# Kernel tuning notes

Hardware: AMD Instinct MI355X
Metric: run time of the kernel (lower is better)

The kernel has to match this reference:

```python
import jax, jax.numpy as jnp
import numpy as np

B, S_IMG, S_TXT, D, H, HD = 1, 2048, 512, 3072, 24, 128
EMB, N_IP = 4096, 64
IP_SCALE = 1.0
EPS = 1e-6
SM_SCALE = 1.0 / np.sqrt(HD).astype(np.float32)


def _lin(x, W, b=None):
    # torch Linear: y = x @ W.T + b, W: [out, in]
    y = jnp.einsum('bsd,od->bso', x, W)
    return y if b is None else y + b


def _heads(x):  # [B,S,D] -> [B,H,S,HD]
    return x.reshape(B, -1, H, HD).transpose(0, 2, 1, 3)


def _rms(x, w):
    return x * jax.lax.rsqrt(jnp.mean(x * x, axis=-1, keepdims=True) + EPS) * w


def _rope(x, cos, sin):
    # interleaved real/imag rotation, cos/sin: [S, HD] broadcast over B,H
    xr = x.reshape(*x.shape[:-1], HD // 2, 2)
    rot = jnp.stack([-xr[..., 1], xr[..., 0]], axis=-1).reshape(x.shape)
    return x * cos + rot * sin


def _sdpa(q, k, v):
    s = jnp.einsum('bhqd,bhkd->bhqk', q, k) * SM_SCALE
    p = jax.nn.softmax(s, axis=-1)
    return jnp.einsum('bhqk,bhkd->bhqd', p, v)


def setup_inputs() -> dict:
    key = jax.random.key(0)
    ks = jax.random.split(key, 32)
    r = lambda i, shape: jax.random.normal(ks[i], shape, dtype=jnp.float32)
    w = lambda i, shape: r(i, shape) * 0.02
    inp = {
        'hidden_states': r(0, (B, S_IMG, D)),
        'encoder_hidden_states': r(1, (B, S_TXT, D)),
        'image_embeds': r(2, (B, N_IP, EMB)),
        'rope_cos': jnp.cos(r(3, (S_TXT + S_IMG, HD))),
        'rope_sin': jnp.sin(r(3, (S_TXT + S_IMG, HD))),
        'Wq': w(4, (D, D)), 'bq': jnp.zeros((D,)),
        'Wk': w(5, (D, D)), 'bk': jnp.zeros((D,)),
        'Wv': w(6, (D, D)), 'bv': jnp.zeros((D,)),
        'Waq': w(7, (D, D)), 'baq': jnp.zeros((D,)),
        'Wak': w(8, (D, D)), 'bak': jnp.zeros((D,)),
        'Wav': w(9, (D, D)), 'bav': jnp.zeros((D,)),
        'Wo': w(10, (D, D)), 'bo': jnp.zeros((D,)),
        'Wao': w(11, (D, D)), 'bao': jnp.zeros((D,)),
        'norm_q_w': jnp.ones((HD,)), 'norm_k_w': jnp.ones((HD,)),
        'norm_aq_w': jnp.ones((HD,)), 'norm_ak_w': jnp.ones((HD,)),
        'Wk_ip': w(12, (D, EMB)), 'Wv_ip': w(13, (D, EMB)),
        'txt_seq_len': S_TXT,
    }
    return inp


def reference(hidden_states, encoder_hidden_states, image_embeds, rope_cos, rope_sin,
              Wq, bq, Wk, bk, Wv, bv, Waq, baq, Wak, bak, Wav, bav,
              Wo, bo, Wao, bao, norm_q_w, norm_k_w, norm_aq_w, norm_ak_w,
              Wk_ip, Wv_ip, txt_seq_len):
    # main stream projections + per-head RMSNorm
    q = _rms(_heads(_lin(hidden_states, Wq, bq)), norm_q_w)
    k = _rms(_heads(_lin(hidden_states, Wk, bk)), norm_k_w)
    v = _heads(_lin(hidden_states, Wv, bv))
    # encoder (text) stream projections + RMSNorm, concat text before image
    eq = _rms(_heads(_lin(encoder_hidden_states, Waq, baq)), norm_aq_w)
    ek = _rms(_heads(_lin(encoder_hidden_states, Wak, bak)), norm_ak_w)
    ev = _heads(_lin(encoder_hidden_states, Wav, bav))
    q = jnp.concatenate([eq, q], axis=2)
    k = jnp.concatenate([ek, k], axis=2)
    v = jnp.concatenate([ev, v], axis=2)
    # IP-adapter branch uses pre-RoPE image-token queries
    ip_q = q[:, :, txt_seq_len:]
    ip_k = _heads(_lin(image_embeds, Wk_ip))
    ip_v = _heads(_lin(image_embeds, Wv_ip))
    ip_hs = _sdpa(ip_q, ip_k, ip_v).transpose(0, 2, 1, 3).reshape(B, -1, H * HD)
    # rotary on joint q/k, then main attention
    q = _rope(q, rope_cos, rope_sin)
    k = _rope(k, rope_cos, rope_sin)
    hs = _sdpa(q, k, v).transpose(0, 2, 1, 3).reshape(B, -1, H * HD)
    # add scaled IP-adapter output to the image part
    img = hs[:, txt_seq_len:] + IP_SCALE * ip_hs
    enc = hs[:, :txt_seq_len]
    # output projections
    out_img = _lin(img, Wo, bo)
    out_enc = _lin(enc, Wao, bao)
    return out_img, out_enc
```

## Files before the change

### kernel.cpp

```cpp
#include <hip/hip_runtime.h>
#include <hip/hip_bf16.h>

#define H 24
#define HD 128
#define DMODEL 3072
#define S_IMG 2048
#define S_TXT 512
#define S_ALL 2560
#define EMB 4096
#define N_IP 64
#define SM_SCALE 0.08838834764831845f

typedef __attribute__((ext_vector_type(8))) short short8;
typedef __attribute__((ext_vector_type(4))) float f32x4;
typedef __attribute__((ext_vector_type(16))) float f32x16;

__device__ inline unsigned short f2bf(float f) {
    unsigned u = __builtin_bit_cast(unsigned, f);
    return (unsigned short)((u + 0x7fffu + ((u >> 16) & 1u)) >> 16);
}
__device__ inline unsigned pk2(float a, float b) {
    return (unsigned)f2bf(a) | ((unsigned)f2bf(b) << 16);
}
__device__ inline float bf2f(unsigned short u) {
    unsigned x = ((unsigned)u) << 16;
    return __builtin_bit_cast(float, x);
}

__device__ inline void gload16(const void* g, void* l) {
    __builtin_amdgcn_global_load_lds(
        (const __attribute__((address_space(1))) unsigned int*)g,
        (__attribute__((address_space(3))) unsigned int*)(unsigned int)(unsigned long long)l,
        16, 0, 0);
}

struct CastSegs {
    const float* src[13];
    unsigned short* dst[13];
    int n8[13];
    int ntot8[13];
    int bstart[14];
};

__global__ __launch_bounds__(256)
void castall(CastSegs cs)
{
    int b = blockIdx.x, seg = 0;
    while (seg < 12 && b >= cs.bstart[seg + 1]) seg++;
    int nb = cs.bstart[seg + 1] - cs.bstart[seg];
    int lb = b - cs.bstart[seg];
    const float* in = cs.src[seg];
    unsigned short* out = cs.dst[seg];
    int n8 = cs.n8[seg], ntot = cs.ntot8[seg];
    for (int i = lb * 256 + threadIdx.x; i < ntot; i += nb * 256) {
        int4 o;
        if (i < n8) {
            const float4* p = (const float4*)(in + (size_t)i * 8);
            float4 a = p[0], bb = p[1];
            o.x = pk2(a.x, a.y); o.y = pk2(a.z, a.w);
            o.z = pk2(bb.x, bb.y); o.w = pk2(bb.z, bb.w);
        } else {
            o.x = 0; o.y = 0; o.z = 0; o.w = 0;
        }
        *(int4*)(out + (size_t)i * 8) = o;
    }
}

__global__ __launch_bounds__(256)
void bcat2(const float* __restrict__ q0, const float* __restrict__ k0, const float* __restrict__ v0,
           const float* __restrict__ q1, const float* __restrict__ k1, const float* __restrict__ v1,
           float* __restrict__ d0, float* __restrict__ d1)
{
    int i = blockIdx.x * 256 + threadIdx.x;
    int which = i >= 3 * DMODEL;
    int j = which ? i - 3 * DMODEL : i;
    const float* a = which ? q1 : q0;
    const float* b = which ? k1 : k0;
    const float* c = which ? v1 : v0;
    float v = (j < DMODEL) ? a[j] : ((j < 2 * DMODEL) ? b[j - DMODEL] : c[j - 2 * DMODEL]);
    (which ? d1 : d0)[j] = v;
}

template<int OUTBF>
__global__ __launch_bounds__(256)
void gemmx(const unsigned short* __restrict__ A0, const unsigned short* __restrict__ B0,
           const float* __restrict__ b0, void* __restrict__ C0,
           const unsigned short* __restrict__ A1, const unsigned short* __restrict__ B1,
           const float* __restrict__ b1, void* __restrict__ C1,
           int mbSplit, int N, int K, int nbm, int GN)
{
    __shared__ unsigned short sm[2 * 8192];
    const int tid = threadIdx.x, lane = tid & 63, wid = tid >> 6;
    const int wr = wid >> 1, wc = wid & 1;
    const int r15 = lane & 15, g = lane >> 4;

    int nwg = gridDim.x;
    int t = (blockIdx.x & 7) * (nwg >> 3) + (blockIdx.x >> 3);
    int gsz = nbm * GN;
    int G = t / gsz, l = t - G * gsz;
    int mb = l % nbm, nb = G * GN + l / nbm;

    const unsigned short* A; const unsigned short* B; const float* bias; void* C; int mrow;
    if (mb < mbSplit) { A = A0; B = B0; bias = b0; C = C0; mrow = mb; }
    else             { A = A1; B = B1; bias = b1; C = C1; mrow = mb - mbSplit; }
    const int m0 = mrow * 128, n0 = nb * 128;

    const int lr = lane >> 3;
    const int lc = lane & 7;
    const int gcol = ((lc * 16) ^ (lr << 4)) >> 1;

    const unsigned short* Ab = A + (size_t)(m0 + wid * 32 + lr) * K + gcol;
    const unsigned short* Bb = B + (size_t)(n0 + wid * 32 + lr) * K + gcol;
    char* smc = (char*)sm;

    f32x4 acc[4][4];
    #pragma unroll
    for (int i = 0; i < 4; i++)
        #pragma unroll
        for (int j = 0; j < 4; j++)
            acc[i][j] = {0.f, 0.f, 0.f, 0.f};

    for (int k0 = 0; k0 < K; k0 += 64) {
        #pragma unroll
        for (int cc = 0; cc < 4; cc++) {
            gload16(Ab + (size_t)cc * 8 * K + k0, smc + (wid * 32 + cc * 8) * 128);
            gload16(Bb + (size_t)cc * 8 * K + k0, smc + 16384 + (wid * 32 + cc * 8) * 128);
        }
        __syncthreads();
        #pragma unroll
        for (int ks = 0; ks < 2; ks++) {
            short8 af[4], bf[4];
            #pragma unroll
            for (int mi = 0; mi < 4; mi++) {
                int row = wr * 64 + mi * 16 + r15;
                af[mi] = *(const short8*)(smc + row * 128 + ((ks * 64 + g * 16) ^ ((row & 7) << 4)));
            }
            #pragma unroll
            for (int ni = 0; ni < 4; ni++) {
                int row = wc * 64 + ni * 16 + r15;
                bf[ni] = *(const short8*)(smc + 16384 + row * 128 + ((ks * 64 + g * 16) ^ ((row & 7) << 4)));
            }
            #pragma unroll
            for (int mi = 0; mi < 4; mi++)
                #pragma unroll
                for (int ni = 0; ni < 4; ni++)
                    acc[mi][ni] = __builtin_amdgcn_mfma_f32_16x16x32_bf16(af[mi], bf[ni], acc[mi][ni], 0, 0, 0);
        }
        __syncthreads();
    }
    #pragma unroll
    for (int mi = 0; mi < 4; mi++) {
        #pragma unroll
        for (int ni = 0; ni < 4; ni++) {
            int col = n0 + wc * 64 + ni * 16 + r15;
            float bv = bias ? bias[col] : 0.f;
            #pragma unroll
            for (int r = 0; r < 4; r++) {
                int grow = m0 + wr * 64 + mi * 16 + g * 4 + r;
                float v = acc[mi][ni][r] + bv;
                if (OUTBF)
                    ((unsigned short*)C)[(size_t)grow * N + col] = f2bf(v);
                else
                    ((float*)C)[(size_t)grow * N + col] = v;
            }
        }
    }
}

template<int OUTBF>
__global__ __launch_bounds__(512, 4)
void gemm8(const unsigned short* __restrict__ A0, const unsigned short* __restrict__ B0,
           const float* __restrict__ b0, void* __restrict__ C0,
           const unsigned short* __restrict__ A1, const unsigned short* __restrict__ B1,
           const float* __restrict__ b1, void* __restrict__ C1,
           int mbSplit, int N, int K, int nbn)
{
    __shared__ char sm[73728];
    const int tid = threadIdx.x, lane = tid & 63, wid = tid >> 6;
    const int wm = wid >> 2, wn = wid & 3;
    const int r15 = lane & 15, g = lane >> 4;

    int nwg = gridDim.x;
    int t0 = (blockIdx.x & 7) * (nwg >> 3) + (blockIdx.x >> 3);
    int mb = t0 / nbn, nb = t0 - mb * nbn;

    const unsigned short* A; const unsigned short* B; const float* bias; void* C; int mrow;
    if (mb < mbSplit) { A = A0; B = B0; bias = b0; C = C0; mrow = mb; }
    else              { A = A1; B = B1; bias = b1; C = C1; mrow = mb - mbSplit; }
    const int m0 = mrow * 256, n0 = nb * 128;

    const int fA0 = tid, fA1 = 512 + tid;
    const int rA0 = fA0 >> 2, sA0 = fA0 & 3;
    const int rA1 = fA1 >> 2, sA1 = fA1 & 3;
    const int rB = tid >> 2, sB = tid & 3;
    const unsigned short* Asrc0 = A + (size_t)(m0 + rA0) * K + ((sA0 ^ ((rA0 >> 1) & 3)) << 3);
    const unsigned short* Asrc1 = A + (size_t)(m0 + rA1) * K + ((sA1 ^ ((rA1 >> 1) & 3)) << 3);
    const unsigned short* Bsrc  = B + (size_t)(n0 + rB) * K + ((sB ^ ((rB >> 1) & 3)) << 3);

    f32x4 acc[8][2];
    #pragma unroll
    for (int i = 0; i < 8; i++)
        #pragma unroll
        for (int j = 0; j < 2; j++)
            acc[i][j] = {0.f, 0.f, 0.f, 0.f};

    const int nt = K >> 5;

    auto STAGE = [&](int buf, int kt) {
        char* d = sm + buf * 24576;
        gload16(Asrc0 + (kt << 5), d + fA0 * 16);
        gload16(Asrc1 + (kt << 5), d + fA1 * 16);
        gload16(Bsrc  + (kt << 5), d + 16384 + tid * 16);
    };

    STAGE(0, 0);
    STAGE(1, 1);
    asm volatile("s_waitcnt vmcnt(3)" ::: "memory");
    __builtin_amdgcn_s_barrier();

    int cur = 0, nxt = 2;
    for (int t = 0; t < nt; t++) {
        if (t + 2 < nt) STAGE(nxt, t + 2);
        const char* As = sm + cur * 24576;
        const char* Bs = As + 16384;
        short8 bfr[2];
        #pragma unroll
        for (int ni = 0; ni < 2; ni++) {
            int brow = wn * 32 + ni * 16 + r15;
            bfr[ni] = *(const short8*)(Bs + brow * 64 + ((g ^ ((brow >> 1) & 3)) << 4));
        }
        __builtin_amdgcn_s_setprio(1);
        #pragma unroll
        for (int mi = 0; mi < 8; mi++) {
            int arow = wm * 128 + mi * 16 + r15;
            short8 af = *(const short8*)(As + arow * 64 + ((g ^ ((arow >> 1) & 3)) << 4));
            acc[mi][0] = __builtin_amdgcn_mfma_f32_16x16x32_bf16(af, bfr[0], acc[mi][0], 0, 0, 0);
            acc[mi][1] = __builtin_amdgcn_mfma_f32_16x16x32_bf16(af, bfr[1], acc[mi][1], 0, 0, 0);
        }
        __builtin_amdgcn_s_setprio(0);
        if (t + 1 < nt) {
            if (t + 2 < nt) { asm volatile("s_waitcnt vmcnt(3)" ::: "memory"); }
            else            { asm volatile("s_waitcnt vmcnt(0)" ::: "memory"); }
            __builtin_amdgcn_s_barrier();
        }
        cur = (cur == 2) ? 0 : cur + 1;
        nxt = (nxt == 2) ? 0 : nxt + 1;
    }

    #pragma unroll
    for (int mi = 0; mi < 8; mi++) {
        #pragma unroll
        for (int ni = 0; ni < 2; ni++) {
            int col = n0 + wn * 32 + ni * 16 + r15;
            float bv = bias ? bias[col] : 0.f;
            #pragma unroll
            for (int r = 0; r < 4; r++) {
                int grow = m0 + wm * 128 + mi * 16 + g * 4 + r;
                float v = acc[mi][ni][r] + bv;
                if (OUTBF)
                    ((unsigned short*)C)[(size_t)grow * N + col] = f2bf(v);
                else
                    ((float*)C)[(size_t)grow * N + col] = v;
            }
        }
    }
}

__global__ __launch_bounds__(256)
void rmsropeQK(const unsigned short* __restrict__ qkvb,
               const float* __restrict__ nqw, const float* __restrict__ nkw,
               const float* __restrict__ naqw, const float* __restrict__ nakw,
               const float* __restrict__ cosb, const float* __restrict__ sinb,
               unsigned short* __restrict__ qb, unsigned short* __restrict__ kb,
               unsigned short* __restrict__ ipq)
{
    int wg = blockIdx.x * 4 + (threadIdx.x >> 6);
    int lane = threadIdx.x & 63;
    int s = wg / H, h = wg - s * H;
    const unsigned short* row = qkvb + (size_t)s * (3 * DMODEL);
    unsigned uq = *(const unsigned*)(row + h * HD + lane * 2);
    unsigned uk = *(const unsigned*)(row + DMODEL + h * HD + lane * 2);
    float q0 = bf2f((unsigned short)uq), q1 = bf2f((unsigned short)(uq >> 16));
    float k0 = bf2f((unsigned short)uk), k1 = bf2f((unsigned short)(uk >> 16));
    float sq = q0 * q0 + q1 * q1, sk = k0 * k0 + k1 * k1;
    #pragma unroll
    for (int off = 1; off < 64; off <<= 1) {
        sq += __shfl_xor(sq, off);
        sk += __shfl_xor(sk, off);
    }
    float rq = rsqrtf(sq * (1.f / HD) + 1e-6f) * SM_SCALE;
    float rk = rsqrtf(sk * (1.f / HD) + 1e-6f);
    const float* wq = (s < S_TXT) ? naqw : nqw;
    const float* wk = (s < S_TXT) ? nakw : nkw;
    float xq0 = q0 * rq * wq[lane * 2], xq1 = q1 * rq * wq[lane * 2 + 1];
    float xk0 = k0 * rk * wk[lane * 2], xk1 = k1 * rk * wk[lane * 2 + 1];
    if (s >= S_TXT)
        *(unsigned*)(ipq + (size_t)h * S_IMG * HD + (size_t)(s - S_TXT) * HD + lane * 2) = pk2(xq0, xq1);
    float c0 = cosb[s * HD + lane * 2], c1 = cosb[s * HD + lane * 2 + 1];
    float s0 = sinb[s * HD + lane * 2], s1 = sinb[s * HD + lane * 2 + 1];
    *(unsigned*)(qb + (size_t)h * S_ALL * HD + (size_t)s * HD + lane * 2) =
        pk2(xq0 * c0 - xq1 * s0, xq1 * c1 + xq0 * s1);
    *(unsigned*)(kb + (size_t)h * S_ALL * HD + (size_t)s * HD + lane * 2) =
        pk2(xk0 * c0 - xk1 * s0, xk1 * c1 + xk0 * s1);
}

__global__ __launch_bounds__(256)
void vtrans(const unsigned short* __restrict__ src, int stride,
            unsigned short* __restrict__ vt, int Stot)
{
    __shared__ unsigned short lv[64 * 130];
    int h = blockIdx.y;
    int s0 = blockIdx.x * 64;
    const unsigned short* base = src + (size_t)s0 * stride + h * HD;
    int tid = threadIdx.x;
    #pragma unroll
    for (int i = 0; i < 4; i++) {
        int slot = tid + 256 * i;
        int row = slot >> 4, c = slot & 15;
        int4 v = *(const int4*)(base + (size_t)row * stride + c * 8);
        unsigned* p = (unsigned*)(lv + row * 130 + c * 8);
        p[0] = (unsigned)v.x; p[1] = (unsigned)v.y; p[2] = (unsigned)v.z; p[3] = (unsigned)v.w;
    }
    __syncthreads();
    #pragma unroll
    for (int i = 0; i < 4; i++) {
        int slot = tid + 256 * i;
        int d = slot >> 3, c8 = slot & 7;
        unsigned w0 = lv[(c8 * 8 + 0) * 130 + d] | ((unsigned)lv[(c8 * 8 + 1) * 130 + d] << 16);
        unsigned w1 = lv[(c8 * 8 + 2) * 130 + d] | ((unsigned)lv[(c8 * 8 + 3) * 130 + d] << 16);
        unsigned w2 = lv[(c8 * 8 + 4) * 130 + d] | ((unsigned)lv[(c8 * 8 + 5) * 130 + d] << 16);
        unsigned w3 = lv[(c8 * 8 + 6) * 130 + d] | ((unsigned)lv[(c8 * 8 + 7) * 130 + d] << 16);
        int4 o = {(int)w0, (int)w1, (int)w2, (int)w3};
        *(int4*)(vt + (size_t)(h * HD + d) * Stot + s0 + c8 * 8) = o;
    }
}

__global__ __launch_bounds__(256)
void cast_heads8(const unsigned short* __restrict__ in, unsigned short* __restrict__ out)
{
    int idx = blockIdx.x * 256 + threadIdx.x;
    int s = idx / 384;
    int rem = idx - s * 384;
    int h = rem >> 4, d8 = rem & 15;
    int4 v = *(const int4*)(in + (size_t)s * (2 * DMODEL) + h * HD + d8 * 8);
    *(int4*)(out + ((size_t)h * N_IP + s) * HD + d8 * 8) = v;
}

template<int MODE, int KVBLK>
__global__ __launch_bounds__(512, 2)
void flash4(const unsigned short* __restrict__ Q, const unsigned short* __restrict__ Kb,
            const unsigned short* __restrict__ Vt, const unsigned short* __restrict__ ipb,
            unsigned short* __restrict__ Out, int Sq, int Skv)
{
    __shared__ char sm[66560];
    const int h = blockIdx.y;
    const int q0 = blockIdx.x * 256;
    const int tid = threadIdx.x, w = tid >> 6, lane = tid & 63;
    const int l31 = lane & 31, hi = lane >> 5;
    const int T2 = KVBLK / 32, K4 = KVBLK / 16, SLOTV = KVBLK / 8, NL = KVBLK / 32;
    const int VROWB = KVBLK * 2;

    const unsigned short* Qh = Q + ((size_t)h * Sq + q0 + w * 32 + l31) * HD + hi * 8;
    short8 qf[8];
    #pragma unroll
    for (int c = 0; c < 8; c++)
        qf[c] = *(const short8*)(Qh + c * 16);

    float m = -3.0e38f, lsum = 0.f;
    f32x16 o[4];
    #pragma unroll
    for (int dn = 0; dn < 4; dn++)
        #pragma unroll
        for (int r = 0; r < 16; r++) o[dn][r] = 0.f;

    const unsigned short* Kh = Kb + (size_t)h * Skv * HD;
    const unsigned short* Vth = Vt + (size_t)h * HD * Skv;
    float* scl = (float*)(sm + 65536) + w * 32;
    const int nt = Skv / KVBLK;

    for (int t = 0; t < nt; t++) {
        int kv0 = t * KVBLK;
        #pragma unroll
        for (int cc = 0; cc < NL; cc++) {
            int f = cc * 512 + tid;
            int row = f >> 4, slot = f & 15;
            gload16(Kh + (size_t)(kv0 + row) * HD + (((slot * 16) ^ ((row & 7) << 4)) >> 1),
                    sm + f * 16);
        }
        #pragma unroll
        for (int cc = 0; cc < NL; cc++) {
            int f = cc * 512 + tid;
            int d = f / SLOTV, slot = f % SLOTV;
            gload16(Vth + (size_t)d * Skv + kv0 + (((slot * 16) ^ ((d & 7) << 4)) >> 1),
                    sm + 32768 + f * 16);
        }
        __syncthreads();

        f32x16 st[T2];
        __builtin_amdgcn_s_setprio(1);
        #pragma unroll
        for (int t2 = 0; t2 < T2; t2++) {
            #pragma unroll
            for (int r = 0; r < 16; r++) st[t2][r] = 0.f;
            #pragma unroll
            for (int c = 0; c < 8; c++) {
                int krow = t2 * 32 + l31;
                short8 kf = *(const short8*)(sm + krow * 256 + ((c * 32 + hi * 16) ^ ((krow & 7) << 4)));
                st[t2] = __builtin_amdgcn_mfma_f32_32x32x16_bf16(kf, qf[c], st[t2], 0, 0, 0);
            }
        }
        __builtin_amdgcn_s_setprio(0);

        float pmax = st[0][0];
        #pragma unroll
        for (int t2 = 0; t2 < T2; t2++)
            #pragma unroll
            for (int r = 0; r < 16; r++) pmax = fmaxf(pmax, st[t2][r]);
        pmax = fmaxf(pmax, __shfl_xor(pmax, 32));

        if (!__all(pmax - m <= 8.0f)) {
            float mn = fmaxf(m, pmax);
            float sc = __expf(m - mn);
            m = mn;
            lsum *= sc;
            if (hi == 0) scl[l31] = sc;
            float scb[16];
            #pragma unroll
            for (int r = 0; r < 16; r++)
                scb[r] = scl[(r & 3) + 8 * (r >> 2) + 4 * hi];
            #pragma unroll
            for (int dn = 0; dn < 4; dn++)
                #pragma unroll
                for (int r = 0; r < 16; r++) o[dn][r] *= scb[r];
        }

        float psum = 0.f;
        #pragma unroll
        for (int t2 = 0; t2 < T2; t2++)
            #pragma unroll
            for (int r = 0; r < 16; r++) {
                float p = __expf(st[t2][r] - m);
                st[t2][r] = p;
                psum += p;
            }
        psum += __shfl_xor(psum, 32);
        lsum += psum;

        short8 pa[K4];
        #pragma unroll
        for (int k4 = 0; k4 < K4; k4++) {
            unsigned U  = pk2(st[(k4 * 8 + 0) >> 4][(k4 * 8 + 0) & 15], st[(k4 * 8 + 1) >> 4][(k4 * 8 + 1) & 15]);
            unsigned V  = pk2(st[(k4 * 8 + 2) >> 4][(k4 * 8 + 2) & 15], st[(k4 * 8 + 3) >> 4][(k4 * 8 + 3) & 15]);
            unsigned U2 = pk2(st[(k4 * 8 + 4) >> 4][(k4 * 8 + 4) & 15], st[(k4 * 8 + 5) >> 4][(k4 * 8 + 5) & 15]);
            unsigned V2 = pk2(st[(k4 * 8 + 6) >> 4][(k4 * 8 + 6) & 15], st[(k4 * 8 + 7) >> 4][(k4 * 8 + 7) & 15]);
            unsigned SU = __shfl_xor(U, 32), SU2 = __shfl_xor(U2, 32);
            unsigned SV = __shfl_xor(V, 32), SV2 = __shfl_xor(V2, 32);
            uint4 wv;
            wv.x = hi ? SU2 : U;
            wv.y = hi ? SV2 : V;
            wv.z = hi ? U2 : SU;
            wv.w = hi ? V2 : SV;
            pa[k4] = __builtin_bit_cast(short8, wv);
        }

        __builtin_amdgcn_s_setprio(1);
        #pragma unroll
        for (int dn = 0; dn < 4; dn++) {
            #pragma unroll
            for (int k4 = 0; k4 < K4; k4++) {
                int vrow = dn * 32 + l31;
                short8 vf = *(const short8*)(sm + 32768 + vrow * VROWB + ((k4 * 32 + hi * 16) ^ ((vrow & 7) << 4)));
                o[dn] = __builtin_amdgcn_mfma_f32_32x32x16_bf16(pa[k4], vf, o[dn], 0, 0, 0);
            }
        }
        __builtin_amdgcn_s_setprio(0);
        __syncthreads();
    }

    if (hi == 0) scl[l31] = 1.f / lsum;
    float linv[16];
    #pragma unroll
    for (int r = 0; r < 16; r++)
        linv[r] = scl[(r & 3) + 8 * (r >> 2) + 4 * hi];
    #pragma unroll
    for (int dn = 0; dn < 4; dn++) {
        #pragma unroll
        for (int r = 0; r < 16; r++) {
            int qrow = q0 + w * 32 + (r & 3) + 8 * (r >> 2) + 4 * hi;
            int col = h * HD + dn * 32 + l31;
            float val = o[dn][r] * linv[r];
            if (MODE == 1 && qrow >= S_TXT)
                val += bf2f(ipb[(size_t)(qrow - S_TXT) * DMODEL + col]);
            Out[(size_t)qrow * DMODEL + col] = f2bf(val);
        }
    }
}

extern "C" void kernel_launch(void* const* d_in, const int* in_sizes, int n_in,
                              void* d_out, int out_size, void* d_ws, size_t ws_size,
                              hipStream_t stream)
{
    const float* hs   = (const float*)d_in[0];
    const float* enc  = (const float*)d_in[1];
    const float* iemb = (const float*)d_in[2];
    const float* cosb = (const float*)d_in[3];
    const float* sinb = (const float*)d_in[4];
    const float* Wq  = (const float*)d_in[5];  const float* bq  = (const float*)d_in[6];
    const float* Wk  = (const float*)d_in[7];  const float* bk  = (const float*)d_in[8];
    const float* Wv  = (const float*)d_in[9];  const float* bv  = (const float*)d_in[10];
    const float* Waq = (const float*)d_in[11]; const float* baq = (const float*)d_in[12];
    const float* Wak = (const float*)d_in[13]; const float* bak = (const float*)d_in[14];
    const float* Wav = (const float*)d_in[15]; const float* bav = (const float*)d_in[16];
    const float* Wo  = (const float*)d_in[17]; const float* bo  = (const float*)d_in[18];
    const float* Wao = (const float*)d_in[19]; const float* bao = (const float*)d_in[20];
    const float* nq  = (const float*)d_in[21]; const float* nk  = (const float*)d_in[22];
    const float* naq = (const float*)d_in[23]; const float* nak = (const float*)d_in[24];
    const float* Wkip = (const float*)d_in[25]; const float* Wvip = (const float*)d_in[26];
    (void)in_sizes; (void)n_in; (void)out_size; (void)ws_size;

    char* ws = (char*)d_ws;
    size_t off = 0;
    auto alloc = [&](size_t b) { char* p = ws + off; off += (b + 255) & ~(size_t)255; return p; };
    unsigned short* qkvb    = (unsigned short*)alloc((size_t)S_ALL * 3 * DMODEL * 2);
    unsigned short* ipkvb   = (unsigned short*)alloc((size_t)128 * 2 * DMODEL * 2);
    unsigned short* hs_bf   = (unsigned short*)alloc((size_t)S_IMG * DMODEL * 2);
    unsigned short* enc_bf  = (unsigned short*)alloc((size_t)S_TXT * DMODEL * 2);
    unsigned short* iemb_bf = (unsigned short*)alloc((size_t)128 * EMB * 2);
    unsigned short* Wqkv  = (unsigned short*)alloc((size_t)3 * DMODEL * DMODEL * 2);
    unsigned short* Waqkv = (unsigned short*)alloc((size_t)3 * DMODEL * DMODEL * 2);
    unsigned short* Wo_b  = (unsigned short*)alloc((size_t)DMODEL * DMODEL * 2);
    unsigned short* Wao_b = (unsigned short*)alloc((size_t)DMODEL * DMODEL * 2);
    unsigned short* Wip   = (unsigned short*)alloc((size_t)2 * DMODEL * EMB * 2);
    float* bqkv  = (float*)alloc(3 * DMODEL * 4);
    float* baqkv = (float*)alloc(3 * DMODEL * 4);
    unsigned short* qb    = (unsigned short*)alloc((size_t)H * S_ALL * HD * 2);
    unsigned short* kbf   = (unsigned short*)alloc((size_t)H * S_ALL * HD * 2);
    unsigned short* vtb   = (unsigned short*)alloc((size_t)H * HD * S_ALL * 2);
    unsigned short* ipqb  = (unsigned short*)alloc((size_t)H * S_IMG * HD * 2);
    unsigned short* ipkb  = (unsigned short*)alloc((size_t)H * N_IP * HD * 2);
    unsigned short* ipvtb = (unsigned short*)alloc((size_t)H * HD * N_IP * 2);
    unsigned short* ipbuf = (unsigned short*)alloc((size_t)S_IMG * DMODEL * 2);
    unsigned short* attnb = (unsigned short*)alloc((size_t)S_ALL * DMODEL * 2);

    const size_t DD = (size_t)DMODEL * DMODEL;
    const size_t DE = (size_t)DMODEL * EMB;
    const int D8 = (int)(DD / 8), E8 = (int)(DE / 8);

    CastSegs cs;
    const float* srcs[13] = {hs, enc, iemb, Wq, Wk, Wv, Waq, Wak, Wav, Wo, Wao, Wkip, Wvip};
    unsigned short* dsts[13] = {hs_bf, enc_bf, iemb_bf,
                                Wqkv, Wqkv + DD, Wqkv + 2 * DD,
                                Waqkv, Waqkv + DD, Waqkv + 2 * DD,
                                Wo_b, Wao_b, Wip, Wip + DE};
    int n8s[13]  = {S_IMG * DMODEL / 8, S_TXT * DMODEL / 8, N_IP * EMB / 8,
                    D8, D8, D8, D8, D8, D8, D8, D8, E8, E8};
    int nt8s[13] = {S_IMG * DMODEL / 8, S_TXT * DMODEL / 8, 128 * EMB / 8,
                    D8, D8, D8, D8, D8, D8, D8, D8, E8, E8};
    int acc = 0;
    for (int i = 0; i < 13; i++) {
        cs.src[i] = srcs[i]; cs.dst[i] = dsts[i];
        cs.n8[i] = n8s[i]; cs.ntot8[i] = nt8s[i];
        cs.bstart[i] = acc;
        int nb = (nt8s[i] + 8191) / 8192;
        acc += (nb < 1 ? 1 : nb);
    }
    cs.bstart[13] = acc;

    dim3 blk(256);
    castall<<<dim3(acc), blk, 0, stream>>>(cs);
    bcat2<<<dim3(72), blk, 0, stream>>>(bq, bk, bv, baq, bak, bav, bqkv, baqkv);

    gemm8<1><<<dim3(720), dim3(512), 0, stream>>>(
        hs_bf, Wqkv, bqkv, qkvb + (size_t)S_TXT * 3 * DMODEL,
        enc_bf, Waqkv, baqkv, qkvb,
        8, 3 * DMODEL, DMODEL, 72);
    gemmx<1><<<dim3(48), blk, 0, stream>>>(
        iemb_bf, Wip, nullptr, ipkvb,
        iemb_bf, Wip, nullptr, ipkvb,
        1, 2 * DMODEL, EMB, 1, 6);

    rmsropeQK<<<dim3(15360), blk, 0, stream>>>(qkvb, nq, nk, naq, nak, cosb, sinb, qb, kbf, ipqb);
    vtrans<<<dim3(40, 24), blk, 0, stream>>>(qkvb + 2 * DMODEL, 3 * DMODEL, vtb, S_ALL);
    cast_heads8<<<dim3(96), blk, 0, stream>>>(ipkvb, ipkb);
    vtrans<<<dim3(1, 24), blk, 0, stream>>>(ipkvb + DMODEL, 2 * DMODEL, ipvtb, N_IP);

    dim3 fblk(512);
    flash4<0, 64><<<dim3(8, 24),  fblk, 0, stream>>>(ipqb, ipkb, ipvtb, nullptr, ipbuf, S_IMG, N_IP);
    flash4<1, 128><<<dim3(10, 24), fblk, 0, stream>>>(qb, kbf, vtb, ipbuf, attnb, S_ALL, S_ALL);

    float* dout = (float*)d_out;
    gemm8<0><<<dim3(240), dim3(512), 0, stream>>>(
        attnb + (size_t)S_TXT * DMODEL, Wo_b, bo, dout,
        attnb, Wao_b, bao, dout + (size_t)S_IMG * DMODEL,
        8, DMODEL, DMODEL, 24);
}
```

Before: 634.7 us.

## Fuse fp32-to-bf16 weight cast into GEMM B loads; double-buffer flash attention

The GEMM now reads the fp32 projection weights straight into registers, converts them to bf16 and writes them to shared memory. This removes the separate cast pass over the eight D×D weights and its bf16 copies. The K loop is unrolled by two with explicit register staging, and the A tiles still use async global-to-LDS loads. The flash kernel switches to a fixed 64-wide KV block with double-buffered LDS staging, so the next tile loads while the current one computes. The trade-off is twice the global bytes for B in the GEMMs, since each weight tile is reread as fp32 by every M block. The main flash kernel also drops from 128- to 64-wide KV blocks.

```diff
diff --git a/kernel.cpp b/kernel.cpp
--- a/kernel.cpp
+++ b/kernel.cpp
@@ -35,18 +35,18 @@
 }
 
 struct CastSegs {
-    const float* src[13];
-    unsigned short* dst[13];
-    int n8[13];
-    int ntot8[13];
-    int bstart[14];
+    const float* src[5];
+    unsigned short* dst[5];
+    int n8[5];
+    int ntot8[5];
+    int bstart[6];
 };
 
 __global__ __launch_bounds__(256)
 void castall(CastSegs cs)
 {
     int b = blockIdx.x, seg = 0;
-    while (seg < 12 && b >= cs.bstart[seg + 1]) seg++;
+    while (seg < 4 && b >= cs.bstart[seg + 1]) seg++;
     int nb = cs.bstart[seg + 1] - cs.bstart[seg];
     int lb = b - cs.bstart[seg];
     const float* in = cs.src[seg];
@@ -167,13 +167,13 @@
     }
 }
 
+struct BPtr { const float* w[3]; };
+
 template<int OUTBF>
 __global__ __launch_bounds__(512, 4)
-void gemm8(const unsigned short* __restrict__ A0, const unsigned short* __restrict__ B0,
-           const float* __restrict__ b0, void* __restrict__ C0,
-           const unsigned short* __restrict__ A1, const unsigned short* __restrict__ B1,
-           const float* __restrict__ b1, void* __restrict__ C1,
-           int mbSplit, int N, int K, int nbn)
+void gemm8f(const unsigned short* __restrict__ A0, BPtr B0, const float* __restrict__ b0, void* __restrict__ C0,
+            const unsigned short* __restrict__ A1, BPtr B1, const float* __restrict__ b1, void* __restrict__ C1,
+            int mbSplit, int N, int K, int nbn)
 {
     __shared__ char sm[73728];
     const int tid = threadIdx.x, lane = tid & 63, wid = tid >> 6;
@@ -184,9 +184,9 @@
     int t0 = (blockIdx.x & 7) * (nwg >> 3) + (blockIdx.x >> 3);
     int mb = t0 / nbn, nb = t0 - mb * nbn;
 
-    const unsigned short* A; const unsigned short* B; const float* bias; void* C; int mrow;
-    if (mb < mbSplit) { A = A0; B = B0; bias = b0; C = C0; mrow = mb; }
-    else              { A = A1; B = B1; bias = b1; C = C1; mrow = mb - mbSplit; }
+    const unsigned short* A; BPtr Bp; const float* bias; void* C; int mrow;
+    if (mb < mbSplit) { A = A0; Bp = B0; bias = b0; C = C0; mrow = mb; }
+    else              { A = A1; Bp = B1; bias = b1; C = C1; mrow = mb - mbSplit; }
     const int m0 = mrow * 256, n0 = nb * 128;
 
     const int fA0 = tid, fA1 = 512 + tid;
@@ -195,7 +195,9 @@
     const int rB = tid >> 2, sB = tid & 3;
     const unsigned short* Asrc0 = A + (size_t)(m0 + rA0) * K + ((sA0 ^ ((rA0 >> 1) & 3)) << 3);
     const unsigned short* Asrc1 = A + (size_t)(m0 + rA1) * K + ((sA1 ^ ((rA1 >> 1) & 3)) << 3);
-    const unsigned short* Bsrc  = B + (size_t)(n0 + rB) * K + ((sB ^ ((rB >> 1) & 3)) << 3);
+    int bi = nb / 24;
+    int brow0 = (nb - bi * 24) * 128;
+    const float* Bf = Bp.w[bi] + (size_t)(brow0 + rB) * K + ((sB ^ ((rB >> 1) & 3)) << 3);
 
     f32x4 acc[8][2];
     #pragma unroll
@@ -205,24 +207,24 @@
             acc[i][j] = {0.f, 0.f, 0.f, 0.f};
 
     const int nt = K >> 5;
-
-    auto STAGE = [&](int buf, int kt) {
-        char* d = sm + buf * 24576;
+    float4 bvA[2], bvB[2];
+
+    auto STAGEA = [&](char* d, int kt) {
         gload16(Asrc0 + (kt << 5), d + fA0 * 16);
         gload16(Asrc1 + (kt << 5), d + fA1 * 16);
-        gload16(Bsrc  + (kt << 5), d + 16384 + tid * 16);
     };
-
-    STAGE(0, 0);
-    STAGE(1, 1);
-    asm volatile("s_waitcnt vmcnt(3)" ::: "memory");
-    __builtin_amdgcn_s_barrier();
-
-    int cur = 0, nxt = 2;
-    for (int t = 0; t < nt; t++) {
-        if (t + 2 < nt) STAGE(nxt, t + 2);
-        const char* As = sm + cur * 24576;
-        const char* Bs = As + 16384;
+    auto LOADB = [&](float4* bv, int kt) {
+        bv[0] = *(const float4*)(Bf + (kt << 5));
+        bv[1] = *(const float4*)(Bf + (kt << 5) + 4);
+    };
+    auto CVTW = [&](char* d, const float4* bv) {
+        int4 o;
+        o.x = pk2(bv[0].x, bv[0].y); o.y = pk2(bv[0].z, bv[0].w);
+        o.z = pk2(bv[1].x, bv[1].y); o.w = pk2(bv[1].z, bv[1].w);
+        *(int4*)(d + 16384 + tid * 16) = o;
+    };
+    auto COMPUTE = [&](const char* P) {
+        const char* Bs = P + 16384;
         short8 bfr[2];
         #pragma unroll
         for (int ni = 0; ni < 2; ni++) {
@@ -233,18 +235,45 @@
         #pragma unroll
         for (int mi = 0; mi < 8; mi++) {
             int arow = wm * 128 + mi * 16 + r15;
-            short8 af = *(const short8*)(As + arow * 64 + ((g ^ ((arow >> 1) & 3)) << 4));
+            short8 af = *(const short8*)(P + arow * 64 + ((g ^ ((arow >> 1) & 3)) << 4));
             acc[mi][0] = __builtin_amdgcn_mfma_f32_16x16x32_bf16(af, bfr[0], acc[mi][0], 0, 0, 0);
             acc[mi][1] = __builtin_amdgcn_mfma_f32_16x16x32_bf16(af, bfr[1], acc[mi][1], 0, 0, 0);
         }
         __builtin_amdgcn_s_setprio(0);
-        if (t + 1 < nt) {
-            if (t + 2 < nt) { asm volatile("s_waitcnt vmcnt(3)" ::: "memory"); }
-            else            { asm volatile("s_waitcnt vmcnt(0)" ::: "memory"); }
+    };
+
+    char* Pa = sm;
+    char* Pb = sm + 24576;
+    char* Pc = sm + 49152;
+
+    STAGEA(Pa, 0); LOADB(bvA, 0);
+    STAGEA(Pb, 1); LOADB(bvB, 1);
+    asm volatile("s_waitcnt vmcnt(4)" ::: "memory");
+    CVTW(Pa, bvA);
+    asm volatile("s_waitcnt lgkmcnt(0)" ::: "memory");
+    __builtin_amdgcn_s_barrier();
+
+    for (int t = 0; t < nt; t += 2) {
+        bool s2 = (t + 2 < nt);
+        if (s2) { STAGEA(Pc, t + 2); LOADB(bvA, t + 2); }
+        COMPUTE(Pa);
+        if (s2) { asm volatile("s_waitcnt vmcnt(4)" ::: "memory"); }
+        else    { asm volatile("s_waitcnt vmcnt(0)" ::: "memory"); }
+        CVTW(Pb, bvB);
+        asm volatile("s_waitcnt lgkmcnt(0)" ::: "memory");
+        __builtin_amdgcn_s_barrier();
+        { char* tmp = Pa; Pa = Pb; Pb = Pc; Pc = tmp; }
+        bool s3 = (t + 3 < nt);
+        if (s3) { STAGEA(Pc, t + 3); LOADB(bvB, t + 3); }
+        COMPUTE(Pa);
+        if (s2) {
+            if (s3) { asm volatile("s_waitcnt vmcnt(4)" ::: "memory"); }
+            else    { asm volatile("s_waitcnt vmcnt(0)" ::: "memory"); }
+            CVTW(Pb, bvA);
+            asm volatile("s_waitcnt lgkmcnt(0)" ::: "memory");
             __builtin_amdgcn_s_barrier();
         }
-        cur = (cur == 2) ? 0 : cur + 1;
-        nxt = (nxt == 2) ? 0 : nxt + 1;
+        { char* tmp = Pa; Pa = Pb; Pb = Pc; Pc = tmp; }
     }
 
     #pragma unroll
@@ -346,9 +375,9 @@
     *(int4*)(out + ((size_t)h * N_IP + s) * HD + d8 * 8) = v;
 }
 
-template<int MODE, int KVBLK>
+template<int MODE>
 __global__ __launch_bounds__(512, 2)
-void flash4(const unsigned short* __restrict__ Q, const unsigned short* __restrict__ Kb,
+void flash5(const unsigned short* __restrict__ Q, const unsigned short* __restrict__ Kb,
             const unsigned short* __restrict__ Vt, const unsigned short* __restrict__ ipb,
             unsigned short* __restrict__ Out, int Sq, int Skv)
 {
@@ -357,8 +386,6 @@
     const int q0 = blockIdx.x * 256;
     const int tid = threadIdx.x, w = tid >> 6, lane = tid & 63;
     const int l31 = lane & 31, hi = lane >> 5;
-    const int T2 = KVBLK / 32, K4 = KVBLK / 16, SLOTV = KVBLK / 8, NL = KVBLK / 32;
-    const int VROWB = KVBLK * 2;
 
     const unsigned short* Qh = Q + ((size_t)h * Sq + q0 + w * 32 + l31) * HD + hi * 8;
     short8 qf[8];
@@ -376,36 +403,45 @@
     const unsigned short* Kh = Kb + (size_t)h * Skv * HD;
     const unsigned short* Vth = Vt + (size_t)h * HD * Skv;
     float* scl = (float*)(sm + 65536) + w * 32;
-    const int nt = Skv / KVBLK;
-
-    for (int t = 0; t < nt; t++) {
-        int kv0 = t * KVBLK;
-        #pragma unroll
-        for (int cc = 0; cc < NL; cc++) {
+    const int nt = Skv >> 6;
+
+    auto STAGE = [&](char* base, int kv0) {
+        #pragma unroll
+        for (int cc = 0; cc < 2; cc++) {
             int f = cc * 512 + tid;
             int row = f >> 4, slot = f & 15;
             gload16(Kh + (size_t)(kv0 + row) * HD + (((slot * 16) ^ ((row & 7) << 4)) >> 1),
-                    sm + f * 16);
-        }
-        #pragma unroll
-        for (int cc = 0; cc < NL; cc++) {
+                    base + f * 16);
+        }
+        #pragma unroll
+        for (int cc = 0; cc < 2; cc++) {
             int f = cc * 512 + tid;
-            int d = f / SLOTV, slot = f % SLOTV;
+            int d = f >> 3, slot = f & 7;
             gload16(Vth + (size_t)d * Skv + kv0 + (((slot * 16) ^ ((d & 7) << 4)) >> 1),
-                    sm + 32768 + f * 16);
-        }
-        __syncthreads();
-
-        f32x16 st[T2];
+                    base + 16384 + f * 16);
+        }
+    };
+
+    STAGE(sm, 0);
+    __syncthreads();
+
+    for (int t = 0; t < nt; t++) {
+        char* cur = (t & 1) ? (sm + 32768) : sm;
+        char* oth = (t & 1) ? sm : (sm + 32768);
+        if (t + 1 < nt) STAGE(oth, (t + 1) * 64);
+        const char* Ks = cur;
+        const char* Vs = cur + 16384;
+
+        f32x16 st[2];
         __builtin_amdgcn_s_setprio(1);
         #pragma unroll
-        for (int t2 = 0; t2 < T2; t2++) {
+        for (int t2 = 0; t2 < 2; t2++) {
             #pragma unroll
             for (int r = 0; r < 16; r++) st[t2][r] = 0.f;
             #pragma unroll
             for (int c = 0; c < 8; c++) {
                 int krow = t2 * 32 + l31;
-                short8 kf = *(const short8*)(sm + krow * 256 + ((c * 32 + hi * 16) ^ ((krow & 7) << 4)));
+                short8 kf = *(const short8*)(Ks + krow * 256 + ((c * 32 + hi * 16) ^ ((krow & 7) << 4)));
                 st[t2] = __builtin_amdgcn_mfma_f32_32x32x16_bf16(kf, qf[c], st[t2], 0, 0, 0);
             }
         }
@@ -413,7 +449,7 @@
 
         float pmax = st[0][0];
         #pragma unroll
-        for (int t2 = 0; t2 < T2; t2++)
+        for (int t2 = 0; t2 < 2; t2++)
             #pragma unroll
             for (int r = 0; r < 16; r++) pmax = fmaxf(pmax, st[t2][r]);
         pmax = fmaxf(pmax, __shfl_xor(pmax, 32));
@@ -436,7 +472,7 @@
 
         float psum = 0.f;
         #pragma unroll
-        for (int t2 = 0; t2 < T2; t2++)
+        for (int t2 = 0; t2 < 2; t2++)
             #pragma unroll
             for (int r = 0; r < 16; r++) {
                 float p = __expf(st[t2][r] - m);
@@ -446,9 +482,9 @@
         psum += __shfl_xor(psum, 32);
         lsum += psum;
 
-        short8 pa[K4];
-        #pragma unroll
-        for (int k4 = 0; k4 < K4; k4++) {
+        short8 pa[4];
+        #pragma unroll
+        for (int k4 = 0; k4 < 4; k4++) {
             unsigned U  = pk2(st[(k4 * 8 + 0) >> 4][(k4 * 8 + 0) & 15], st[(k4 * 8 + 1) >> 4][(k4 * 8 + 1) & 15]);
             unsigned V  = pk2(st[(k4 * 8 + 2) >> 4][(k4 * 8 + 2) & 15], st[(k4 * 8 + 3) >> 4][(k4 * 8 + 3) & 15]);
             unsigned U2 = pk2(st[(k4 * 8 + 4) >> 4][(k4 * 8 + 4) & 15], st[(k4 * 8 + 5) >> 4][(k4 * 8 + 5) & 15]);
@@ -467,9 +503,9 @@
         #pragma unroll
         for (int dn = 0; dn < 4; dn++) {
             #pragma unroll
-            for (int k4 = 0; k4 < K4; k4++) {
+            for (int k4 = 0; k4 < 4; k4++) {
                 int vrow = dn * 32 + l31;
-                short8 vf = *(const short8*)(sm + 32768 + vrow * VROWB + ((k4 * 32 + hi * 16) ^ ((vrow & 7) << 4)));
+                short8 vf = *(const short8*)(Vs + vrow * 128 + ((k4 * 32 + hi * 16) ^ ((vrow & 7) << 4)));
                 o[dn] = __builtin_amdgcn_mfma_f32_32x32x16_bf16(pa[k4], vf, o[dn], 0, 0, 0);
             }
         }
@@ -526,10 +562,6 @@
     unsigned short* hs_bf   = (unsigned short*)alloc((size_t)S_IMG * DMODEL * 2);
     unsigned short* enc_bf  = (unsigned short*)alloc((size_t)S_TXT * DMODEL * 2);
     unsigned short* iemb_bf = (unsigned short*)alloc((size_t)128 * EMB * 2);
-    unsigned short* Wqkv  = (unsigned short*)alloc((size_t)3 * DMODEL * DMODEL * 2);
-    unsigned short* Waqkv = (unsigned short*)alloc((size_t)3 * DMODEL * DMODEL * 2);
-    unsigned short* Wo_b  = (unsigned short*)alloc((size_t)DMODEL * DMODEL * 2);
-    unsigned short* Wao_b = (unsigned short*)alloc((size_t)DMODEL * DMODEL * 2);
     unsigned short* Wip   = (unsigned short*)alloc((size_t)2 * DMODEL * EMB * 2);
     float* bqkv  = (float*)alloc(3 * DMODEL * 4);
     float* baqkv = (float*)alloc(3 * DMODEL * 4);
@@ -542,37 +574,36 @@
     unsigned short* ipbuf = (unsigned short*)alloc((size_t)S_IMG * DMODEL * 2);
     unsigned short* attnb = (unsigned short*)alloc((size_t)S_ALL * DMODEL * 2);
 
-    const size_t DD = (size_t)DMODEL * DMODEL;
     const size_t DE = (size_t)DMODEL * EMB;
-    const int D8 = (int)(DD / 8), E8 = (int)(DE / 8);
+    const int E8 = (int)(DE / 8);
 
     CastSegs cs;
-    const float* srcs[13] = {hs, enc, iemb, Wq, Wk, Wv, Waq, Wak, Wav, Wo, Wao, Wkip, Wvip};
-    unsigned short* dsts[13] = {hs_bf, enc_bf, iemb_bf,
-                                Wqkv, Wqkv + DD, Wqkv + 2 * DD,
-                                Waqkv, Waqkv + DD, Waqkv + 2 * DD,
-                                Wo_b, Wao_b, Wip, Wip + DE};
-    int n8s[13]  = {S_IMG * DMODEL / 8, S_TXT * DMODEL / 8, N_IP * EMB / 8,
-                    D8, D8, D8, D8, D8, D8, D8, D8, E8, E8};
-    int nt8s[13] = {S_IMG * DMODEL / 8, S_TXT * DMODEL / 8, 128 * EMB / 8,
-                    D8, D8, D8, D8, D8, D8, D8, D8, E8, E8};
+    const float* srcs[5] = {hs, enc, iemb, Wkip, Wvip};
+    unsigned short* dsts[5] = {hs_bf, enc_bf, iemb_bf, Wip, Wip + DE};
+    int n8s[5]  = {S_IMG * DMODEL / 8, S_TXT * DMODEL / 8, N_IP * EMB / 8, E8, E8};
+    int nt8s[5] = {S_IMG * DMODEL / 8, S_TXT * DMODEL / 8, 128 * EMB / 8, E8, E8};
     int acc = 0;
-    for (int i = 0; i < 13; i++) {
+    for (int i = 0; i < 5; i++) {
         cs.src[i] = srcs[i]; cs.dst[i] = dsts[i];
         cs.n8[i] = n8s[i]; cs.ntot8[i] = nt8s[i];
         cs.bstart[i] = acc;
         int nb = (nt8s[i] + 8191) / 8192;
         acc += (nb < 1 ? 1 : nb);
     }
-    cs.bstart[13] = acc;
+    cs.bstart[5] = acc;
 
     dim3 blk(256);
     castall<<<dim3(acc), blk, 0, stream>>>(cs);
     bcat2<<<dim3(72), blk, 0, stream>>>(bq, bk, bv, baq, bak, bav, bqkv, baqkv);
 
-    gemm8<1><<<dim3(720), dim3(512), 0, stream>>>(
-        hs_bf, Wqkv, bqkv, qkvb + (size_t)S_TXT * 3 * DMODEL,
-        enc_bf, Waqkv, baqkv, qkvb,
+    BPtr Bqkv  = {{Wq, Wk, Wv}};
+    BPtr Baqkv = {{Waq, Wak, Wav}};
+    BPtr Bo    = {{Wo, nullptr, nullptr}};
+    BPtr Bao   = {{Wao, nullptr, nullptr}};
+
+    gemm8f<1><<<dim3(720), dim3(512), 0, stream>>>(
+        hs_bf, Bqkv, bqkv, qkvb + (size_t)S_TXT * 3 * DMODEL,
+        enc_bf, Baqkv, baqkv, qkvb,
         8, 3 * DMODEL, DMODEL, 72);
     gemmx<1><<<dim3(48), blk, 0, stream>>>(
         iemb_bf, Wip, nullptr, ipkvb,
@@ -585,12 +616,12 @@
     vtrans<<<dim3(1, 24), blk, 0, stream>>>(ipkvb + DMODEL, 2 * DMODEL, ipvtb, N_IP);
 
     dim3 fblk(512);
-    flash4<0, 64><<<dim3(8, 24),  fblk, 0, stream>>>(ipqb, ipkb, ipvtb, nullptr, ipbuf, S_IMG, N_IP);
-    flash4<1, 128><<<dim3(10, 24), fblk, 0, stream>>>(qb, kbf, vtb, ipbuf, attnb, S_ALL, S_ALL);
+    flash5<0><<<dim3(8, 24),  fblk, 0, stream>>>(ipqb, ipkb, ipvtb, nullptr, ipbuf, S_IMG, N_IP);
+    flash5<1><<<dim3(10, 24), fblk, 0, stream>>>(qb, kbf, vtb, ipbuf, attnb, S_ALL, S_ALL);
 
     float* dout = (float*)d_out;
-    gemm8<0><<<dim3(240), dim3(512), 0, stream>>>(
-        attnb + (size_t)S_TXT * DMODEL, Wo_b, bo, dout,
-        attnb, Wao_b, bao, dout + (size_t)S_IMG * DMODEL,
+    gemm8f<0><<<dim3(240), dim3(512), 0, stream>>>(
+        attnb + (size_t)S_TXT * DMODEL, Bo, bo, dout,
+        attnb, Bao, bao, dout + (size_t)S_IMG * DMODEL,
         8, DMODEL, DMODEL, 24);
 }
```

Result: slower. 749.7 us (+18.1%).

## Double-buffer flash attention KV tiles and shrink GEMM to two-stage buffering

Applied to the files above, without the earlier changes.

The flash attention kernel now uses a fixed 64-row KV block and loads the next K/V tile into a second shared-memory buffer while computing on the current one, so global loads overlap with MFMA work. The GEMM drops from triple to double buffering, cutting shared memory and raising the launch-bounds occupancy hint, but it now waits for all outstanding loads each iteration. The main attention loses its larger 128-row KV tile, which means more iterations and more barriers. The GEMM prefetch distance is shorter, which may expose more load latency.

```diff
diff --git a/kernel.cpp b/kernel.cpp
--- a/kernel.cpp
+++ b/kernel.cpp
@@ -168,14 +168,14 @@
 }
 
 template<int OUTBF>
-__global__ __launch_bounds__(512, 4)
+__global__ __launch_bounds__(512, 6)
 void gemm8(const unsigned short* __restrict__ A0, const unsigned short* __restrict__ B0,
            const float* __restrict__ b0, void* __restrict__ C0,
            const unsigned short* __restrict__ A1, const unsigned short* __restrict__ B1,
            const float* __restrict__ b1, void* __restrict__ C1,
            int mbSplit, int N, int K, int nbn)
 {
-    __shared__ char sm[73728];
+    __shared__ char sm[49152];
     const int tid = threadIdx.x, lane = tid & 63, wid = tid >> 6;
     const int wm = wid >> 2, wn = wid & 3;
     const int r15 = lane & 15, g = lane >> 4;
@@ -206,23 +206,22 @@
 
     const int nt = K >> 5;
 
-    auto STAGE = [&](int buf, int kt) {
-        char* d = sm + buf * 24576;
+    auto STAGE = [&](char* d, int kt) {
         gload16(Asrc0 + (kt << 5), d + fA0 * 16);
         gload16(Asrc1 + (kt << 5), d + fA1 * 16);
         gload16(Bsrc  + (kt << 5), d + 16384 + tid * 16);
     };
 
-    STAGE(0, 0);
-    STAGE(1, 1);
-    asm volatile("s_waitcnt vmcnt(3)" ::: "memory");
+    STAGE(sm, 0);
+    asm volatile("s_waitcnt vmcnt(0)" ::: "memory");
     __builtin_amdgcn_s_barrier();
 
-    int cur = 0, nxt = 2;
     for (int t = 0; t < nt; t++) {
-        if (t + 2 < nt) STAGE(nxt, t + 2);
-        const char* As = sm + cur * 24576;
-        const char* Bs = As + 16384;
+        char* cur = sm + (t & 1) * 24576;
+        char* oth = sm + ((t + 1) & 1) * 24576;
+        if (t + 1 < nt) STAGE(oth, t + 1);
+        const char* As = cur;
+        const char* Bs = cur + 16384;
         short8 bfr[2];
         #pragma unroll
         for (int ni = 0; ni < 2; ni++) {
@@ -238,13 +237,8 @@
             acc[mi][1] = __builtin_amdgcn_mfma_f32_16x16x32_bf16(af, bfr[1], acc[mi][1], 0, 0, 0);
         }
         __builtin_amdgcn_s_setprio(0);
-        if (t + 1 < nt) {
-            if (t + 2 < nt) { asm volatile("s_waitcnt vmcnt(3)" ::: "memory"); }
-            else            { asm volatile("s_waitcnt vmcnt(0)" ::: "memory"); }
-            __builtin_amdgcn_s_barrier();
-        }
-        cur = (cur == 2) ? 0 : cur + 1;
-        nxt = (nxt == 2) ? 0 : nxt + 1;
+        asm volatile("s_waitcnt vmcnt(0)" ::: "memory");
+        __builtin_amdgcn_s_barrier();
     }
 
     #pragma unroll
@@ -346,9 +340,9 @@
     *(int4*)(out + ((size_t)h * N_IP + s) * HD + d8 * 8) = v;
 }
 
-template<int MODE, int KVBLK>
+template<int MODE>
 __global__ __launch_bounds__(512, 2)
-void flash4(const unsigned short* __restrict__ Q, const unsigned short* __restrict__ Kb,
+void flash5(const unsigned short* __restrict__ Q, const unsigned short* __restrict__ Kb,
             const unsigned short* __restrict__ Vt, const unsigned short* __restrict__ ipb,
             unsigned short* __restrict__ Out, int Sq, int Skv)
 {
@@ -357,8 +351,6 @@
     const int q0 = blockIdx.x * 256;
     const int tid = threadIdx.x, w = tid >> 6, lane = tid & 63;
     const int l31 = lane & 31, hi = lane >> 5;
-    const int T2 = KVBLK / 32, K4 = KVBLK / 16, SLOTV = KVBLK / 8, NL = KVBLK / 32;
-    const int VROWB = KVBLK * 2;
 
     const unsigned short* Qh = Q + ((size_t)h * Sq + q0 + w * 32 + l31) * HD + hi * 8;
     short8 qf[8];
@@ -376,36 +368,45 @@
     const unsigned short* Kh = Kb + (size_t)h * Skv * HD;
     const unsigned short* Vth = Vt + (size_t)h * HD * Skv;
     float* scl = (float*)(sm + 65536) + w * 32;
-    const int nt = Skv / KVBLK;
-
-    for (int t = 0; t < nt; t++) {
-        int kv0 = t * KVBLK;
-        #pragma unroll
-        for (int cc = 0; cc < NL; cc++) {
+    const int nt = Skv >> 6;
+
+    auto STAGE = [&](char* base, int kv0) {
+        #pragma unroll
+        for (int cc = 0; cc < 2; cc++) {
             int f = cc * 512 + tid;
             int row = f >> 4, slot = f & 15;
             gload16(Kh + (size_t)(kv0 + row) * HD + (((slot * 16) ^ ((row & 7) << 4)) >> 1),
-                    sm + f * 16);
-        }
-        #pragma unroll
-        for (int cc = 0; cc < NL; cc++) {
+                    base + f * 16);
+        }
+        #pragma unroll
+        for (int cc = 0; cc < 2; cc++) {
             int f = cc * 512 + tid;
-            int d = f / SLOTV, slot = f % SLOTV;
+            int d = f >> 3, slot = f & 7;
             gload16(Vth + (size_t)d * Skv + kv0 + (((slot * 16) ^ ((d & 7) << 4)) >> 1),
-                    sm + 32768 + f * 16);
-        }
-        __syncthreads();
-
-        f32x16 st[T2];
+                    base + 16384 + f * 16);
+        }
+    };
+
+    STAGE(sm, 0);
+    __syncthreads();
+
+    for (int t = 0; t < nt; t++) {
+        char* cur = (t & 1) ? (sm + 32768) : sm;
+        char* oth = (t & 1) ? sm : (sm + 32768);
+        if (t + 1 < nt) STAGE(oth, (t + 1) * 64);
+        const char* Ks = cur;
+        const char* Vs = cur + 16384;
+
+        f32x16 st[2];
         __builtin_amdgcn_s_setprio(1);
         #pragma unroll
-        for (int t2 = 0; t2 < T2; t2++) {
+        for (int t2 = 0; t2 < 2; t2++) {
             #pragma unroll
             for (int r = 0; r < 16; r++) st[t2][r] = 0.f;
             #pragma unroll
             for (int c = 0; c < 8; c++) {
                 int krow = t2 * 32 + l31;
-                short8 kf = *(const short8*)(sm + krow * 256 + ((c * 32 + hi * 16) ^ ((krow & 7) << 4)));
+                short8 kf = *(const short8*)(Ks + krow * 256 + ((c * 32 + hi * 16) ^ ((krow & 7) << 4)));
                 st[t2] = __builtin_amdgcn_mfma_f32_32x32x16_bf16(kf, qf[c], st[t2], 0, 0, 0);
             }
         }
@@ -413,7 +414,7 @@
 
         float pmax = st[0][0];
         #pragma unroll
-        for (int t2 = 0; t2 < T2; t2++)
+        for (int t2 = 0; t2 < 2; t2++)
             #pragma unroll
             for (int r = 0; r < 16; r++) pmax = fmaxf(pmax, st[t2][r]);
         pmax = fmaxf(pmax, __shfl_xor(pmax, 32));
@@ -436,7 +437,7 @@
 
         float psum = 0.f;
         #pragma unroll
-        for (int t2 = 0; t2 < T2; t2++)
+        for (int t2 = 0; t2 < 2; t2++)
             #pragma unroll
             for (int r = 0; r < 16; r++) {
                 float p = __expf(st[t2][r] - m);
@@ -446,9 +447,9 @@
         psum += __shfl_xor(psum, 32);
         lsum += psum;
 
-        short8 pa[K4];
-        #pragma unroll
-        for (int k4 = 0; k4 < K4; k4++) {
+        short8 pa[4];
+        #pragma unroll
+        for (int k4 = 0; k4 < 4; k4++) {
             unsigned U  = pk2(st[(k4 * 8 + 0) >> 4][(k4 * 8 + 0) & 15], st[(k4 * 8 + 1) >> 4][(k4 * 8 + 1) & 15]);
             unsigned V  = pk2(st[(k4 * 8 + 2) >> 4][(k4 * 8 + 2) & 15], st[(k4 * 8 + 3) >> 4][(k4 * 8 + 3) & 15]);
             unsigned U2 = pk2(st[(k4 * 8 + 4) >> 4][(k4 * 8 + 4) & 15], st[(k4 * 8 + 5) >> 4][(k4 * 8 + 5) & 15]);
@@ -467,9 +468,9 @@
         #pragma unroll
         for (int dn = 0; dn < 4; dn++) {
             #pragma unroll
-            for (int k4 = 0; k4 < K4; k4++) {
+            for (int k4 = 0; k4 < 4; k4++) {
                 int vrow = dn * 32 + l31;
-                short8 vf = *(const short8*)(sm + 32768 + vrow * VROWB + ((k4 * 32 + hi * 16) ^ ((vrow & 7) << 4)));
+                short8 vf = *(const short8*)(Vs + vrow * 128 + ((k4 * 32 + hi * 16) ^ ((vrow & 7) << 4)));
                 o[dn] = __builtin_amdgcn_mfma_f32_32x32x16_bf16(pa[k4], vf, o[dn], 0, 0, 0);
             }
         }
@@ -585,8 +586,8 @@
     vtrans<<<dim3(1, 24), blk, 0, stream>>>(ipkvb + DMODEL, 2 * DMODEL, ipvtb, N_IP);
 
     dim3 fblk(512);
-    flash4<0, 64><<<dim3(8, 24),  fblk, 0, stream>>>(ipqb, ipkb, ipvtb, nullptr, ipbuf, S_IMG, N_IP);
-    flash4<1, 128><<<dim3(10, 24), fblk, 0, stream>>>(qb, kbf, vtb, ipbuf, attnb, S_ALL, S_ALL);
+    flash5<0><<<dim3(8, 24),  fblk, 0, stream>>>(ipqb, ipkb, ipvtb, nullptr, ipbuf, S_IMG, N_IP);
+    flash5<1><<<dim3(10, 24), fblk, 0, stream>>>(qb, kbf, vtb, ipbuf, attnb, S_ALL, S_ALL);
 
     float* dout = (float*)d_out;
     gemm8<0><<<dim3(240), dim3(512), 0, stream>>>(
```

New measurement: 1.229 ms. 93.7% more time.
